# Kernel optimization log

Hardware: AMD Instinct MI355X
Metric: run time of the kernel (lower is better)

The kernel has to match this reference:

```python
import jax, jax.numpy as jnp
import numpy as np

N, F, T, E, TS, H = 10000, 64, 8, 160000, 200, 128
K = max(1, int(N * 0.5))
EPS = 1e-8


def layer_norm(x, g, b):
    m = x.mean(-1, keepdims=True)
    v = ((x - m) ** 2).mean(-1, keepdims=True)
    return (x - m) * jax.lax.rsqrt(v + 1e-5) * g + b


def setup_inputs() -> dict:
    key = jax.random.key(0)
    ks = jax.random.split(key, 16)
    s = lambda i, shape, scale=0.05: jax.random.normal(ks[i], shape, jnp.float32) * scale
    return {
        "x_seq": jax.random.normal(ks[0], (T, N, F), jnp.float32),
        "h0": jnp.zeros((N, H), jnp.float32),
        "c0": jnp.zeros((N, H), jnp.float32),
        "time_series": jax.random.normal(ks[1], (TS, N), jnp.float32),
        "Wx": s(2, (4, H, F)),            # gate order: input, forget, output, modulation
        "bx": jnp.zeros((4, H), jnp.float32),
        "Wh": s(3, (4, H, H)),
        "bh": jnp.zeros((4, H), jnp.float32),
        "ln_mod_g": jnp.ones((H,), jnp.float32),
        "ln_mod_b": jnp.zeros((H,), jnp.float32),
        "map_W": s(4, (3, H, H)),         # p1_i0, p2_i0, p2_i1
        "pool_vec": jax.random.normal(ks[5], (H, 1), jnp.float32),
        "lstm_Wih": s(6, (4 * H, N), 0.01),
        "lstm_Whh": s(7, (4 * H, H)),
        "lstm_bih": jnp.zeros((4 * H,), jnp.float32),
        "lstm_bhh": jnp.zeros((4 * H,), jnp.float32),
        "mlp_W1": s(8, (H, 2 * H)),
        "mlp_b1": jnp.zeros((H,), jnp.float32),
        "mlp_ln_g": jnp.ones((H,), jnp.float32),
        "mlp_ln_b": jnp.zeros((H,), jnp.float32),
        "mlp_W2": s(9, (H // 2, H)),
        "mlp_b2": jnp.zeros((H // 2,), jnp.float32),
        "mlp_W3": s(10, (1, H // 2)),
        "mlp_b3": jnp.zeros((1,), jnp.float32),
        "edge_index": jax.random.randint(ks[11], (2, E), 0, N, jnp.int32),
    }


def _forward(x_seq, h0, c0, time_series, Wx, bx, Wh, bh, ln_mod_g, ln_mod_b,
             map_W, pool_vec, lstm_Wih, lstm_Whh, lstm_bih, lstm_bhh,
             mlp_W1, mlp_b1, mlp_ln_g, mlp_ln_b, mlp_W2, mlp_b2, mlp_W3, mlp_b3,
             edge_index):
    src, dst = edge_index[0], edge_index[1]
    # GCN symmetric norm with self-loops: D^{-1/2}(A+I)D^{-1/2}
    deg = 1.0 + jax.ops.segment_sum(jnp.ones((E,), jnp.float32), dst, num_segments=N)
    dis = jax.lax.rsqrt(deg)
    enorm = dis[src] * dis[dst]
    self_norm = dis * dis

    def aggregate(hfeat):  # one shared gather/scatter for all 4 gates, [N, 4H]
        out = jax.ops.segment_sum(hfeat[src] * enorm[:, None], dst, num_segments=N)
        return out + hfeat * self_norm[:, None]

    bias = (bx + bh).reshape(4 * H)

    def cell(x, h, c):
        lin = (jnp.einsum('nf,ghf->ngh', x, Wx).reshape(N, 4 * H)
               + jnp.einsum('nd,ghd->ngh', h, Wh).reshape(N, 4 * H))
        pre = (aggregate(lin) + bias).reshape(N, 4, H)  # aggregation is linear -> fuse x- and h-branches
        i = jax.nn.relu(pre[:, 0])
        f = jax.nn.relu(pre[:, 1])
        o = jax.nn.relu(pre[:, 2])
        g = jnp.tanh(layer_norm(pre[:, 3], ln_mod_g, ln_mod_b))
        c_new = f * c + i * g
        return o * jnp.tanh(c_new), c_new

    # jump_connection_parallel over strides p in {1, 2}
    last = []
    for p in (1, 2):
        for off in range(p):
            h, c = h0, c0
            for t in range(off, T, p):
                h, c = cell(x_seq[t], h, c)
            last.append(h)
    hidden = sum(last[j] @ map_W[j].T for j in range(3))  # p1_i0 + p2_i0 + p2_i1

    # DGPool
    v = pool_vec / (jnp.linalg.norm(pool_vec) + EPS)
    sc = (hidden @ v).squeeze(-1)
    sc = (sc - sc.mean()) / (sc.std() + EPS)
    sig = jax.nn.sigmoid(sc)
    x_scaled = hidden * sig[:, None]
    _, idx = jax.lax.top_k(sig, K)
    new_x = x_scaled[idx]
    ss = -jnp.sort(-sig)
    pool_loss = -(jnp.log(ss[:K] + EPS).sum() + jnp.log(1.0 - ss[K:] + EPS).sum()) / N
    high = new_x.mean(axis=0)

    # raw time-series LSTM (torch gate order i, f, g, o)
    def step(carry, x_t):
        hh, cc = carry
        z = lstm_Wih @ x_t + lstm_bih + lstm_Whh @ hh + lstm_bhh
        i_, f_, g_, o_ = jnp.split(z, 4)
        cc = jax.nn.sigmoid(f_) * cc + jax.nn.sigmoid(i_) * jnp.tanh(g_)
        return (jax.nn.sigmoid(o_) * jnp.tanh(cc), cc), None

    (h_last, _), _ = jax.lax.scan(step, (jnp.zeros(H, jnp.float32), jnp.zeros(H, jnp.float32)), time_series)

    fusion = jnp.concatenate([high, h_last])
    m = jax.nn.relu(mlp_W1 @ fusion + mlp_b1)
    m = layer_norm(m, mlp_ln_g, mlp_ln_b)      # dropout = identity (eval mode)
    m = jax.nn.relu(mlp_W2 @ m + mlp_b2)
    pred = mlp_W3 @ m + mlp_b3
    return pred, pool_loss


def reference(x_seq, h0, c0, time_series, Wx, bx, Wh, bh, ln_mod_g, ln_mod_b,
              map_W, pool_vec, lstm_Wih, lstm_Whh, lstm_bih, lstm_bhh,
              mlp_W1, mlp_b1, mlp_ln_g, mlp_ln_b, mlp_W2, mlp_b2, mlp_W3, mlp_b3,
              edge_index):
    return _forward(x_seq, h0, c0, time_series, Wx, bx, Wh, bh, ln_mod_g, ln_mod_b,
                    map_W, pool_vec, lstm_Wih, lstm_Whh, lstm_bih, lstm_bhh,
                    mlp_W1, mlp_b1, mlp_ln_g, mlp_ln_b, mlp_W2, mlp_b2, mlp_W3, mlp_b3,
                    edge_index)
```

## Files before the change

### kernel.cpp

```cpp
#include <hip/hip_runtime.h>
#include <hip/hip_bf16.h>
#include <math.h>

#define NN 10000
#define FF 64
#define TSTEPS 8
#define EE 160000
#define TSS 200
#define HH 128
#define KK 5000
#define G4 512
#define KIN 192
#define EPSF 1e-8f

typedef __attribute__((ext_vector_type(8))) short short8v;
typedef __attribute__((ext_vector_type(4))) float f32x4;

__device__ inline float wred(float v){
  #pragma unroll
  for (int off = 32; off > 0; off >>= 1) v += __shfl_xor(v, off);
  return v;
}

__device__ inline unsigned short f2b(float f) {
  union { __hip_bfloat16 h; unsigned short u; } cv;
  cv.h = __float2bfloat16(f);
  return cv.u;
}
__device__ inline float b2f(unsigned short u) {
  return __uint_as_float(((unsigned int)u) << 16);
}


__global__ void k_setup_w(const float* Wx, const float* Wh, const float* bx, const float* bh,
                          const float* mapW, unsigned short* Wfrag, float* biasC, float* mapWr) {
  int idx = blockIdx.x * 256 + threadIdx.x;
  {
    int jj = idx & 7, l = (idx >> 3) & 63, ntg = (idx >> 9) & 31, ks = idx >> 14;
    int k = ks * 32 + ((l >> 4) << 3) + jj;
    int gh = ntg * 16 + (l & 15);
    int g = gh >> 7, hh = gh & 127;
    float v = (k < FF) ? Wx[(g * HH + hh) * FF + k] : Wh[(g * HH + hh) * HH + (k - FF)];
    Wfrag[idx] = f2b(v);
  }
  if (idx < G4) biasC[idx] = bx[idx] + bh[idx];
  if (idx < 3 * HH * HH) {
    int s = idx / (HH * HH), r = idx % (HH * HH);
    int d = r / HH, j = r % HH;
    mapWr[idx] = mapW[(s * HH + j) * HH + d];
  }
}

__global__ void k_zero(int* deg, int* cursor, int* rank, float* acc, float* high) {
  int i = blockIdx.x * 256 + threadIdx.x;
  if (i < NN) { deg[i] = 0; cursor[i] = 0; rank[i] = 0; }
  if (i < 16) acc[i] = 0.f;
  if (i < 128) high[i] = 0.f;
}

__global__ void k_deg(const int* ei, int* deg) {
  int e = blockIdx.x * 256 + threadIdx.x;
  if (e < EE) atomicAdd(&deg[ei[EE + e]], 1);
}

__global__ void k_norm(const int* deg, float* dis, float* self_norm) {
  int n = blockIdx.x * 256 + threadIdx.x;
  if (n < NN) {
    float d = 1.0f + (float)deg[n];
    dis[n] = rsqrtf(d);
    self_norm[n] = 1.0f / d;
  }
}

__global__ void k_scan(const int* deg, int* row_ptr, int n) {
  __shared__ int buf[1024];
  __shared__ int carry;
  if (threadIdx.x == 0) carry = 0;
  __syncthreads();
  for (int base = 0; base < n; base += 1024) {
    int i = base + threadIdx.x;
    int v = (i < n) ? deg[i] : 0;
    buf[threadIdx.x] = v;
    __syncthreads();
    for (int off = 1; off < 1024; off <<= 1) {
      int t = (threadIdx.x >= off) ? buf[threadIdx.x - off] : 0;
      __syncthreads();
      buf[threadIdx.x] += t;
      __syncthreads();
    }
    if (i < n) row_ptr[i] = carry + buf[threadIdx.x] - v;
    __syncthreads();
    if (threadIdx.x == 1023) carry += buf[1023];
    __syncthreads();
  }
  if (threadIdx.x == 0) row_ptr[n] = carry;
}

__global__ void k_fill(const int* ei, const int* row_ptr, int* cursor, const float* dis,
                       int* col_src, float* col_w) {
  int e = blockIdx.x * 256 + threadIdx.x;
  if (e < EE) {
    int s = ei[e], d = ei[EE + e];
    int pos = row_ptr[d] + atomicAdd(&cursor[d], 1);
    col_src[pos] = s;
    col_w[pos] = dis[s] * dis[d];
  }
}

__global__ void k_init3(const float* h0, const float* c0, unsigned short* hAll, float* cAll) {
  int i = blockIdx.x * 256 + threadIdx.x;
  if (i < NN * HH) {
    unsigned short h = f2b(h0[i]);
    float c = c0[i];
    hAll[i] = h; hAll[NN * HH + i] = h; hAll[2 * NN * HH + i] = h;
    cAll[i] = c; cAll[NN * HH + i] = c; cAll[2 * NN * HH + i] = c;
  }
}

__global__ void k_xcast(const float* x, unsigned short* xb) {
  int i = blockIdx.x * 256 + threadIdx.x;
  float4 v = *(const float4*)(x + (size_t)i * 4);
  ushort4 u;
  u.x = f2b(v.x); u.y = f2b(v.y); u.z = f2b(v.z); u.w = f2b(v.w);
  *(ushort4*)(xb + (size_t)i * 4) = u;
}


__global__ void __launch_bounds__(256) k_aggx8(const unsigned short* xb, const int* row_ptr,
    const int* col_src, const float* col_w, const float* self_n, unsigned short* aggX) {
  __shared__ int es[4][64];
  __shared__ float ew[4][64];
  int wv = threadIdx.x >> 6, lane = threadIdx.x & 63;
  int p = blockIdx.x * 4 + wv;
  int t = p / NN, n = p - t * NN;
  int e0 = row_ptr[n], e1 = row_ptr[n + 1];
  float acc = 0.f;
  for (int eb = e0; eb < e1; eb += 64) {
    int cnt = min(64, e1 - eb);
    if (lane < cnt) { es[wv][lane] = col_src[eb + lane]; ew[wv][lane] = col_w[eb + lane]; }
    __builtin_amdgcn_wave_barrier();
    for (int i = 0; i < cnt; i++)
      acc += b2f(xb[((size_t)t * NN + es[wv][i]) * FF + lane]) * ew[wv][i];
    __builtin_amdgcn_wave_barrier();
  }
  acc += b2f(xb[((size_t)t * NN + n) * FF + lane]) * self_n[n];
  aggX[(size_t)p * FF + lane] = f2b(acc);
}

__global__ void __launch_bounds__(256) k_aggh(const unsigned short* hAll, const int* row_ptr,
    const int* col_src, const float* col_w, const float* self_n, unsigned short* aggH, int M) {
  __shared__ int es[4][64];
  __shared__ float ew[4][64];
  int w = threadIdx.x >> 6, lane = threadIdx.x & 63;
  int m = blockIdx.x * 2 + (w >> 1);
  if (m >= M) return;
  int ch = (w & 1) * 64 + lane;
  int c = (m >= 2 * NN) ? 2 : (m >= NN ? 1 : 0);
  int n = m - c * NN;
  int e0 = row_ptr[n], e1 = row_ptr[n + 1];
  const unsigned short* hb = hAll + (size_t)c * NN * HH;
  float acc = 0.f;
  for (int eb = e0; eb < e1; eb += 64) {
    int cnt = min(64, e1 - eb);
    if (lane < cnt) { es[w][lane] = col_src[eb + lane]; ew[w][lane] = col_w[eb + lane]; }
    __builtin_amdgcn_wave_barrier();
    for (int i = 0; i < cnt; i++)
      acc += b2f(hb[(size_t)es[w][i] * HH + ch]) * ew[w][i];
    __builtin_amdgcn_wave_barrier();
  }
  acc += b2f(hAll[(size_t)m * HH + ch]) * self_n[n];
  aggH[(size_t)m * HH + ch] = f2b(acc);
}

__global__ void __launch_bounds__(512) k_premm(const unsigned short* aggX,
    const unsigned short* aggH, const unsigned short* Wfrag, const float* biasC,
    unsigned short* preB, int M, int r) {
  __shared__ unsigned short Af[1536 * 8];
  int m0 = blockIdx.x * 64;
  int n0 = blockIdx.y * 256;
  int tid = threadIdx.x;
  int l = tid & 63, wid = tid >> 6;
  int wm = wid >> 2, wn = wid & 3;
  #pragma unroll
  for (int q = 0; q < 3; q++) {
    int chunk = tid + q * 512;
    int mt = chunk / 384, rem = chunk - mt * 384;
    int ks = rem >> 6, cl = rem & 63;
    int row = m0 + mt * 16 + (cl & 15);
    int kk = ks * 32 + ((cl >> 4) << 3);
    short8v v = {};
    if (row < M) {
      const unsigned short* src;
      if (kk < FF) {
        int ch = (row >= 2 * NN) ? 2 : (row >= NN ? 1 : 0);
        int n = row - ch * NN;
        int t = (ch == 0) ? r : (2 * r + ch - 1);
        src = aggX + ((size_t)t * NN + n) * FF + kk;
      } else {
        src = aggH + (size_t)row * HH + (kk - FF);
      }
      v = *(const short8v*)src;
    }
    *(short8v*)&Af[chunk * 8] = v;
  }
  __syncthreads();
  f32x4 acc[2][4];
  #pragma unroll
  for (int i = 0; i < 2; i++)
    #pragma unroll
    for (int j = 0; j < 4; j++) acc[i][j] = (f32x4){0.f, 0.f, 0.f, 0.f};
  #pragma unroll
  for (int ks = 0; ks < 6; ks++) {
    short8v a0 = *(const short8v*)&Af[(((wm * 2 + 0) * 6 + ks) * 64 + l) * 8];
    short8v a1 = *(const short8v*)&Af[(((wm * 2 + 1) * 6 + ks) * 64 + l) * 8];
    #pragma unroll
    for (int j = 0; j < 4; j++) {
      int ntg = (n0 >> 4) + wn * 4 + j;
      short8v b = *(const short8v*)(Wfrag + (((size_t)ks * 32 + ntg) * 64 + l) * 8);
      acc[0][j] = __builtin_amdgcn_mfma_f32_16x16x32_bf16(a0, b, acc[0][j], 0, 0, 0);
      acc[1][j] = __builtin_amdgcn_mfma_f32_16x16x32_bf16(a1, b, acc[1][j], 0, 0, 0);
    }
  }
  #pragma unroll
  for (int i = 0; i < 2; i++)
    #pragma unroll
    for (int j = 0; j < 4; j++) {
      int colg = n0 + wn * 64 + j * 16 + (l & 15);
      float bv = biasC[colg];
      #pragma unroll
      for (int rg = 0; rg < 4; rg++) {
        int row = m0 + wm * 32 + i * 16 + ((l >> 4) * 4) + rg;
        if (row < M) preB[(size_t)row * G4 + colg] = f2b(acc[i][j][rg] + bv);
      }
    }
}

__global__ void __launch_bounds__(128) k_gates(const unsigned short* preB, const float* lng,
                                               const float* lnb, unsigned short* h, float* c,
                                               int M) {
  int b = blockIdx.x;
  int j = threadIdx.x;
  const unsigned short* p = preB + (size_t)b * G4;
  float iv = b2f(p[j]), fv = b2f(p[128 + j]), ov = b2f(p[256 + j]), gv = b2f(p[384 + j]);
  float s = wred(gv), s2 = wred(gv * gv);
  __shared__ float sh[4];
  int wid = j >> 6;
  if ((j & 63) == 0) { sh[wid] = s; sh[2 + wid] = s2; }
  __syncthreads();
  float mean = (sh[0] + sh[1]) * (1.f / 128.f);
  float var = (sh[2] + sh[3]) * (1.f / 128.f) - mean * mean;
  float gn = (gv - mean) * rsqrtf(var + 1e-5f) * lng[j] + lnb[j];
  float gt = tanhf(gn);
  float ii = fmaxf(iv, 0.f), ff = fmaxf(fv, 0.f), oo = fmaxf(ov, 0.f);
  size_t ci = (size_t)b * HH + j;
  float cn = ff * c[ci] + ii * gt;
  c[ci] = cn;
  h[ci] = f2b(oo * tanhf(cn));
}

__global__ void __launch_bounds__(256) k_hidden(const unsigned short* hA, const unsigned short* hB,
                                                const unsigned short* hC, const float* Wr,
                                                float* out) {
  __shared__ __align__(16) float As[8][128];
  __shared__ __align__(16) float Bs[8][64];
  int m0 = blockIdx.x * 128, n0 = blockIdx.y * 64;
  int tid = threadIdx.x;
  int tx = tid & 15, ty = tid >> 4;
  float acc[8][4] = {};
  for (int kc = 0; kc < 48; kc++) {
    int k0 = kc * 8;
    const unsigned short* S = (k0 < 128) ? hA : (k0 < 256 ? hB : hC);
    int koff = k0 & 127;
    {
      int ml = tid >> 1, kq = (tid & 1) * 4;
      int m = m0 + ml;
      float4 v = make_float4(0.f, 0.f, 0.f, 0.f);
      if (m < NN) {
        ushort4 u = *(const ushort4*)(S + (size_t)m * HH + koff + kq);
        v.x = b2f(u.x); v.y = b2f(u.y); v.z = b2f(u.z); v.w = b2f(u.w);
      }
      As[kq + 0][ml] = v.x; As[kq + 1][ml] = v.y; As[kq + 2][ml] = v.z; As[kq + 3][ml] = v.w;
    }
    #pragma unroll
    for (int q = 0; q < 2; q++) {
      int e = tid + q * 256;
      int kl = e >> 6, nl = e & 63;
      Bs[kl][nl] = Wr[(size_t)(k0 + kl) * HH + n0 + nl];
    }
    __syncthreads();
    #pragma unroll
    for (int k = 0; k < 8; k++) {
      float4 a0 = *(const float4*)&As[k][ty * 4];
      float4 a1 = *(const float4*)&As[k][64 + ty * 4];
      float4 b0 = *(const float4*)&Bs[k][tx * 4];
      const float av0[4] = {a0.x, a0.y, a0.z, a0.w};
      const float av1[4] = {a1.x, a1.y, a1.z, a1.w};
      const float bv[4] = {b0.x, b0.y, b0.z, b0.w};
      #pragma unroll
      for (int i = 0; i < 4; i++)
        #pragma unroll
        for (int j = 0; j < 4; j++) {
          acc[i][j] += av0[i] * bv[j];
          acc[4 + i][j] += av1[i] * bv[j];
        }
    }
    __syncthreads();
  }
  #pragma unroll
  for (int g = 0; g < 2; g++)
    #pragma unroll
    for (int i = 0; i < 4; i++) {
      int m = m0 + g * 64 + ty * 4 + i;
      if (m < NN) {
        float4 r;
        r.x = acc[g * 4 + i][0]; r.y = acc[g * 4 + i][1];
        r.z = acc[g * 4 + i][2]; r.w = acc[g * 4 + i][3];
        *(float4*)(out + (size_t)m * HH + n0 + tx * 4) = r;
      }
    }
}


__global__ void k_vnorm(const float* pv, float* acc) {
  int t = threadIdx.x;
  float v = pv[t];
  float s = wred(v * v);
  __shared__ float sh[2];
  if ((t & 63) == 0) sh[t >> 6] = s;
  __syncthreads();
  if (t == 0) acc[0] = 1.0f / (sqrtf(sh[0] + sh[1]) + EPSF);
}

__global__ void __launch_bounds__(256) k_sc(const float* hidden, const float* pv, float* acc,
                                            float* sc) {
  int wid = threadIdx.x >> 6, lane = threadIdx.x & 63;
  float2 vv = *(const float2*)(pv + lane * 2);
  float inv = acc[0];
  float ls = 0.f, ls2 = 0.f;
  for (int n = blockIdx.x * 4 + wid; n < NN; n += gridDim.x * 4) {
    float2 hv = *(const float2*)(hidden + (size_t)n * HH + lane * 2);
    float dot = hv.x * vv.x + hv.y * vv.y;
    dot = wred(dot);
    if (lane == 0) {
      float s = dot * inv;
      sc[n] = s;
      ls += s;
      ls2 += s * s;
    }
  }
  __shared__ float sh[8];
  if (lane == 0) { sh[wid] = ls; sh[4 + wid] = ls2; }
  __syncthreads();
  if (threadIdx.x == 0) {
    atomicAdd(&acc[1], sh[0] + sh[1] + sh[2] + sh[3]);
    atomicAdd(&acc[2], sh[4] + sh[5] + sh[6] + sh[7]);
  }
}

__global__ void k_sig(const float* sc, const float* acc, float* sig) {
  int n = blockIdx.x * 256 + threadIdx.x;
  if (n < NN) {
    float mean = acc[1] * (1.f / NN);
    float var = acc[2] * (1.f / NN) - mean * mean;
    float sd = sqrtf(fmaxf(var, 0.f)) + EPSF;
    float z = (sc[n] - mean) / sd;
    sig[n] = 1.f / (1.f + expf(-z));
  }
}

__global__ void __launch_bounds__(256) k_rank(const float* sc, int* rank) {
  __shared__ float sj[1024];
  int i = blockIdx.x * 256 + threadIdx.x;
  int j0 = blockIdx.y * 1024;
  for (int k = threadIdx.x; k < 1024; k += 256) {
    int j = j0 + k;
    sj[k] = (j < NN) ? sc[j] : -3.0e38f;
  }
  __syncthreads();
  float si = (i < NN) ? sc[i] : 0.f;
  int jmax = NN - j0; if (jmax > 1024) jmax = 1024;
  int cnt = 0;
  for (int k = 0; k < jmax; k++) {
    float v = sj[k];
    int j = j0 + k;
    cnt += (v > si) || (v == si && j < i);
  }
  if (i < NN && cnt) atomicAdd(&rank[i], cnt);
}

__global__ void __launch_bounds__(256) k_plogs(const float* sig, const int* rank, float* acc) {
  int i = blockIdx.x * 256 + threadIdx.x;
  float v = 0.f;
  if (i < NN) {
    float s = sig[i];
    v = (rank[i] < KK) ? logf(s + EPSF) : logf(1.f - s + EPSF);
  }
  v = wred(v);
  __shared__ float sh[4];
  if ((threadIdx.x & 63) == 0) sh[threadIdx.x >> 6] = v;
  __syncthreads();
  if (threadIdx.x == 0) atomicAdd(&acc[3], sh[0] + sh[1] + sh[2] + sh[3]);
}

__global__ void __launch_bounds__(128) k_high(const float* hidden, const float* sig,
                                              const int* rank, float* high) {
  int ch = threadIdx.x;
  int n0 = blockIdx.x * 128;
  float a = 0.f;
  for (int q = 0; q < 128; q++) {
    int n = n0 + q;
    if (n >= NN) break;
    if (rank[n] < KK) a += hidden[(size_t)n * HH + ch] * sig[n];
  }
  atomicAdd(&high[ch], a);
}


__global__ void __launch_bounds__(256) k_zpre2(const float* Wih, const float* ts, float* part) {
  __shared__ __align__(16) float As[16][64];
  __shared__ __align__(16) float Bs[16][64];
  int m0 = blockIdx.x * 64;
  int n0 = blockIdx.y * 64;
  int ks = blockIdx.z;
  int kbeg = ks * 624;
  int kend = (ks == 15) ? NN : kbeg + 624;
  int tid = threadIdx.x;
  int tx = tid & 15, ty = tid >> 4;
  int lm = tid >> 2, kq = (tid & 3) * 4;
  bool bvalid = (n0 + lm) < TSS;
  float acc[4][4] = {};
  for (int k0 = kbeg; k0 < kend; k0 += 16) {
    {
      float4 v = *(const float4*)(Wih + (size_t)(m0 + lm) * NN + k0 + kq);
      As[kq + 0][lm] = v.x; As[kq + 1][lm] = v.y; As[kq + 2][lm] = v.z; As[kq + 3][lm] = v.w;
    }
    {
      float4 v = make_float4(0.f, 0.f, 0.f, 0.f);
      if (bvalid) v = *(const float4*)(ts + (size_t)(n0 + lm) * NN + k0 + kq);
      Bs[kq + 0][lm] = v.x; Bs[kq + 1][lm] = v.y; Bs[kq + 2][lm] = v.z; Bs[kq + 3][lm] = v.w;
    }
    __syncthreads();
    #pragma unroll
    for (int k = 0; k < 16; k++) {
      float4 a0 = *(const float4*)&As[k][ty * 4];
      float4 b0 = *(const float4*)&Bs[k][tx * 4];
      const float av[4] = {a0.x, a0.y, a0.z, a0.w};
      const float bv[4] = {b0.x, b0.y, b0.z, b0.w};
      #pragma unroll
      for (int i = 0; i < 4; i++)
        #pragma unroll
        for (int j = 0; j < 4; j++)
          acc[i][j] += av[i] * bv[j];
    }
    __syncthreads();
  }
  float* pd = part + ((size_t)ks << 17);
  #pragma unroll
  for (int i = 0; i < 4; i++) {
    float4 r4 = make_float4(acc[i][0], acc[i][1], acc[i][2], acc[i][3]);
    *(float4*)(pd + (size_t)(m0 + ty * 4 + i) * 256 + n0 + tx * 4) = r4;
  }
}

__global__ void __launch_bounds__(256) k_zred(const float* part, float* zpre) {
  int r = blockIdx.x;
  int t = threadIdx.x;
  int base = r * 256 + t;
  float s = 0.f;
  #pragma unroll
  for (int k = 0; k < 16; k++) s += part[(k << 17) + base];
  if (t < TSS) zpre[(size_t)t * G4 + r] = s;
}

__global__ void __launch_bounds__(1024) k_lstm(const float* Whh, const float* bih, const float* bhh,
                                               const float* zpre, float* h_last) {
  __shared__ float part[2][512];
  __shared__ float gact[512];
  int tid = threadIdx.x;
  int half = tid >> 9;
  int r = tid & 511;
  int w = tid >> 6, l = tid & 63;
  float w64[64];
  #pragma unroll
  for (int q = 0; q < 16; q++) {
    float4 v = *(const float4*)(Whh + (size_t)r * HH + 64 * half + 4 * q);
    w64[4 * q + 0] = v.x; w64[4 * q + 1] = v.y;
    w64[4 * q + 2] = v.z; w64[4 * q + 3] = v.w;
  }
  float bias = bih[r] + bhh[r];
  int jbase = (w >= 8) ? 64 : 0;
  float hreg = 0.f, creg = 0.f;
  for (int t = 0; t < TSS; t++) {
    float d = 0.f;
    #pragma unroll
    for (int j = 0; j < 64; j++) {
      float hj = __uint_as_float(__builtin_amdgcn_readlane(__float_as_uint(hreg), j));
      d += w64[j] * hj;
    }
    part[half][r] = d;
    __syncthreads();
    if (tid < 512) {
      float dd = part[0][r] + part[1][r] + bias + zpre[(size_t)t * G4 + r];
      float a = ((r >> 7) == 2) ? tanhf(dd) : (1.f / (1.f + expf(-dd)));
      gact[r] = a;
    }
    __syncthreads();
    int j = jbase + l;
    creg = gact[128 + j] * creg + gact[j] * gact[256 + j];
    hreg = gact[384 + j] * tanhf(creg);
  }
  if (w == 0) h_last[l] = hreg;
  else if (w == 8) h_last[64 + l] = hreg;
}


__global__ void __launch_bounds__(256) k_mlp(const float* high, const float* hlast, const float* acc,
    const float* W1, const float* b1, const float* lng, const float* lnb,
    const float* W2, const float* b2, const float* W3, const float* b3, float* out) {
  __shared__ float fus[256];
  __shared__ float m1[128];
  __shared__ float m2[64];
  __shared__ float red[4];
  int t = threadIdx.x;
  fus[t] = (t < 128) ? high[t] * (1.f / KK) : hlast[t - 128];
  __syncthreads();
  if (t < 128) {
    float a = b1[t];
    for (int k = 0; k < 256; k++) a += W1[t * 256 + k] * fus[k];
    m1[t] = fmaxf(a, 0.f);
  }
  __syncthreads();
  if (t < 128) {
    float x = m1[t];
    float s = wred(x), s2 = wred(x * x);
    if ((t & 63) == 0) { red[t >> 6] = s; red[2 + (t >> 6)] = s2; }
  }
  __syncthreads();
  if (t < 128) {
    float mean = (red[0] + red[1]) * (1.f / 128.f);
    float var = (red[2] + red[3]) * (1.f / 128.f) - mean * mean;
    float xn = (m1[t] - mean) * rsqrtf(var + 1e-5f) * lng[t] + lnb[t];
    __syncthreads();
    m1[t] = xn;
  } else {
    __syncthreads();
  }
  __syncthreads();
  if (t < 64) {
    float a = b2[t];
    for (int k = 0; k < 128; k++) a += W2[t * 128 + k] * m1[k];
    m2[t] = fmaxf(a, 0.f);
  }
  __syncthreads();
  if (t < 64) {
    float a = W3[t] * m2[t];
    a = wred(a);
    if (t == 0) {
      out[0] = a + b3[0];
      out[1] = -acc[3] * (1.f / NN);
    }
  }
}


extern "C" void kernel_launch(void* const* d_in, const int* in_sizes, int n_in,
                              void* d_out, int out_size, void* d_ws, size_t ws_size,
                              hipStream_t stream) {
  const float* x_seq = (const float*)d_in[0];
  const float* h0    = (const float*)d_in[1];
  const float* c0    = (const float*)d_in[2];
  const float* ts    = (const float*)d_in[3];
  const float* Wx    = (const float*)d_in[4];
  const float* bx    = (const float*)d_in[5];
  const float* Wh    = (const float*)d_in[6];
  const float* bh    = (const float*)d_in[7];
  const float* lng   = (const float*)d_in[8];
  const float* lnb   = (const float*)d_in[9];
  const float* mapW  = (const float*)d_in[10];
  const float* pv    = (const float*)d_in[11];
  const float* Wih   = (const float*)d_in[12];
  const float* Whh   = (const float*)d_in[13];
  const float* bih   = (const float*)d_in[14];
  const float* bhh   = (const float*)d_in[15];
  const float* W1    = (const float*)d_in[16];
  const float* b1    = (const float*)d_in[17];
  const float* mlng  = (const float*)d_in[18];
  const float* mlnb  = (const float*)d_in[19];
  const float* W2    = (const float*)d_in[20];
  const float* b2    = (const float*)d_in[21];
  const float* W3    = (const float*)d_in[22];
  const float* b3    = (const float*)d_in[23];
  const int*   ei    = (const int*)d_in[24];

  char* wsp = (char*)d_ws;
  size_t off = 0;
  auto carve = [&](size_t bytes) -> char* {
    char* p = wsp + off;
    off += (bytes + 255) & ~(size_t)255;
    return p;
  };
  unsigned short* Wfrag = (unsigned short*)carve(98304 * 2);
  float* biasC   = (float*)carve(G4 * 4);
  float* mapWr   = (float*)carve(3 * HH * HH * 4);
  int*   degi    = (int*)carve(NN * 4);
  int*   cursor  = (int*)carve(NN * 4);
  int*   rankb   = (int*)carve(NN * 4);
  int*   row_ptr = (int*)carve((NN + 1) * 4);
  float* dis     = (float*)carve(NN * 4);
  float* self_n  = (float*)carve(NN * 4);
  int*   col_src = (int*)carve(EE * 4);
  float* col_w   = (float*)carve(EE * 4);
  unsigned short* hAll = (unsigned short*)carve((size_t)3 * NN * HH * 2);
  float*          cAll = (float*)carve((size_t)3 * NN * HH * 4);
  unsigned short* x2b  = (unsigned short*)carve((size_t)TSTEPS * NN * FF * 2);
  unsigned short* aggX = (unsigned short*)carve((size_t)TSTEPS * NN * FF * 2);
  unsigned short* aggH = (unsigned short*)carve((size_t)3 * NN * HH * 2);
  unsigned short* preB = (unsigned short*)carve((size_t)3 * NN * G4 * 2);
  float* hidden  = (float*)carve((size_t)NN * HH * 4);
  float* sc      = (float*)carve(NN * 4);
  float* sig     = (float*)carve(NN * 4);
  float* acc     = (float*)carve(16 * 4);
  float* high    = (float*)carve(128 * 4);
  float* zpre    = (float*)carve((size_t)TSS * G4 * 4);
  float* hlast   = (float*)carve(128 * 4);

  k_setup_w<<<384, 256, 0, stream>>>(Wx, Wh, bx, bh, mapW, Wfrag, biasC, mapWr);
  k_zero<<<40, 256, 0, stream>>>(degi, cursor, rankb, acc, high);
  k_deg<<<625, 256, 0, stream>>>(ei, degi);
  k_norm<<<40, 256, 0, stream>>>(degi, dis, self_n);
  k_scan<<<1, 1024, 0, stream>>>(degi, row_ptr, NN);
  k_fill<<<625, 256, 0, stream>>>(ei, row_ptr, cursor, dis, col_src, col_w);
  k_init3<<<5000, 256, 0, stream>>>(h0, c0, hAll, cAll);
  k_xcast<<<5000, 256, 0, stream>>>(x_seq, x2b);

  k_aggx8<<<20000, 256, 0, stream>>>(x2b, row_ptr, col_src, col_w, self_n, aggX);

  for (int r = 0; r < TSTEPS; r++) {
    int M = (r < 4) ? 3 * NN : NN;
    k_aggh<<<M / 2, 256, 0, stream>>>(hAll, row_ptr, col_src, col_w, self_n, aggH, M);
    k_premm<<<dim3((M + 63) / 64, 2), 512, 0, stream>>>(aggX, aggH, Wfrag, biasC, preB, M, r);
    k_gates<<<M, 128, 0, stream>>>(preB, lng, lnb, hAll, cAll, M);
  }

  k_hidden<<<dim3(79, 2), 256, 0, stream>>>(hAll, hAll + (size_t)NN * HH,
                                            hAll + (size_t)2 * NN * HH, mapWr, hidden);
  k_vnorm<<<1, 128, 0, stream>>>(pv, acc);
  k_sc<<<250, 256, 0, stream>>>(hidden, pv, acc, sc);
  k_sig<<<40, 256, 0, stream>>>(sc, acc, sig);
  k_rank<<<dim3(40, 10), 256, 0, stream>>>(sc, rankb);
  k_plogs<<<40, 256, 0, stream>>>(sig, rankb, acc);
  k_high<<<79, 128, 0, stream>>>(hidden, sig, rankb, high);

  k_zpre2<<<dim3(8, 4, 16), 256, 0, stream>>>(Wih, ts, (float*)preB);
  k_zred<<<512, 256, 0, stream>>>((float*)preB, zpre);
  k_lstm<<<1, 1024, 0, stream>>>(Whh, bih, bhh, zpre, hlast);

  k_mlp<<<1, 256, 0, stream>>>(high, hlast, acc, W1, b1, mlng, mlnb, W2, b2, W3, b3,
                               (float*)d_out);
}
```

Measured before the change: 1.177 ms.

## Restructure serial LSTM kernel to one thread per gate row with full-row weights

The sequential LSTM recurrence kernel now uses 512 threads, and each thread holds a full 128-wide row of Whh in registers, instead of 1024 threads each holding a half row. This removes the shared-memory partial-sum exchange and one reduction step per timestep. The cell/hidden update now runs on 128 threads and broadcasts h through shared memory. The dot product is split into four independent FMA chains to add ILP. The cost is higher register pressure (128 weight floats per thread) and a serial cell update on two waves, while the block still needs two barriers per step.

```diff
diff --git a/kernel.cpp b/kernel.cpp
--- a/kernel.cpp
+++ b/kernel.cpp
@@ -472,45 +472,52 @@
   if (t < TSS) zpre[(size_t)t * G4 + r] = s;
 }
 
-__global__ void __launch_bounds__(1024) k_lstm(const float* Whh, const float* bih, const float* bhh,
-                                               const float* zpre, float* h_last) {
-  __shared__ float part[2][512];
+#define RLN(x, J) __uint_as_float(__builtin_amdgcn_readlane(__float_as_uint(x), (J)))
+#define MAC4(Q, HR, B, D) \
+  D = fmaf(wv##Q.x, RLN(HR, (B) + 0), D); \
+  D = fmaf(wv##Q.y, RLN(HR, (B) + 1), D); \
+  D = fmaf(wv##Q.z, RLN(HR, (B) + 2), D); \
+  D = fmaf(wv##Q.w, RLN(HR, (B) + 3), D);
+#define LDW(Q) float4 wv##Q = *(const float4*)(wr + 4 * Q);
+
+__global__ void __launch_bounds__(512) k_lstm(const float* Whh, const float* bih, const float* bhh,
+                                              const float* zpre, float* h_last) {
   __shared__ float gact[512];
-  int tid = threadIdx.x;
-  int half = tid >> 9;
-  int r = tid & 511;
-  int w = tid >> 6, l = tid & 63;
-  float w64[64];
-  #pragma unroll
-  for (int q = 0; q < 16; q++) {
-    float4 v = *(const float4*)(Whh + (size_t)r * HH + 64 * half + 4 * q);
-    w64[4 * q + 0] = v.x; w64[4 * q + 1] = v.y;
-    w64[4 * q + 2] = v.z; w64[4 * q + 3] = v.w;
-  }
+  __shared__ float hs[128];
+  int r = threadIdx.x;
+  int l = r & 63;
+  const float* wr = Whh + (size_t)r * HH;
+  LDW(0) LDW(1) LDW(2) LDW(3) LDW(4) LDW(5) LDW(6) LDW(7)
+  LDW(8) LDW(9) LDW(10) LDW(11) LDW(12) LDW(13) LDW(14) LDW(15)
+  LDW(16) LDW(17) LDW(18) LDW(19) LDW(20) LDW(21) LDW(22) LDW(23)
+  LDW(24) LDW(25) LDW(26) LDW(27) LDW(28) LDW(29) LDW(30) LDW(31)
   float bias = bih[r] + bhh[r];
-  int jbase = (w >= 8) ? 64 : 0;
-  float hreg = 0.f, creg = 0.f;
+  float hreg0 = 0.f, hreg1 = 0.f, creg = 0.f;
+  int gate = r >> 7;
   for (int t = 0; t < TSS; t++) {
-    float d = 0.f;
-    #pragma unroll
-    for (int j = 0; j < 64; j++) {
-      float hj = __uint_as_float(__builtin_amdgcn_readlane(__float_as_uint(hreg), j));
-      d += w64[j] * hj;
-    }
-    part[half][r] = d;
-    __syncthreads();
-    if (tid < 512) {
-      float dd = part[0][r] + part[1][r] + bias + zpre[(size_t)t * G4 + r];
-      float a = ((r >> 7) == 2) ? tanhf(dd) : (1.f / (1.f + expf(-dd)));
-      gact[r] = a;
-    }
-    __syncthreads();
-    int j = jbase + l;
-    creg = gact[128 + j] * creg + gact[j] * gact[256 + j];
-    hreg = gact[384 + j] * tanhf(creg);
-  }
-  if (w == 0) h_last[l] = hreg;
-  else if (w == 8) h_last[64 + l] = hreg;
+    float z = zpre[(size_t)t * G4 + r];
+    float d0 = 0.f, d1 = 0.f, d2 = 0.f, d3 = 0.f;
+    MAC4(0, hreg0, 0, d0)  MAC4(1, hreg0, 4, d1)  MAC4(2, hreg0, 8, d2)  MAC4(3, hreg0, 12, d3)
+    MAC4(4, hreg0, 16, d0) MAC4(5, hreg0, 20, d1) MAC4(6, hreg0, 24, d2) MAC4(7, hreg0, 28, d3)
+    MAC4(8, hreg0, 32, d0) MAC4(9, hreg0, 36, d1) MAC4(10, hreg0, 40, d2) MAC4(11, hreg0, 44, d3)
+    MAC4(12, hreg0, 48, d0) MAC4(13, hreg0, 52, d1) MAC4(14, hreg0, 56, d2) MAC4(15, hreg0, 60, d3)
+    MAC4(16, hreg1, 0, d0)  MAC4(17, hreg1, 4, d1)  MAC4(18, hreg1, 8, d2)  MAC4(19, hreg1, 12, d3)
+    MAC4(20, hreg1, 16, d0) MAC4(21, hreg1, 20, d1) MAC4(22, hreg1, 24, d2) MAC4(23, hreg1, 28, d3)
+    MAC4(24, hreg1, 32, d0) MAC4(25, hreg1, 36, d1) MAC4(26, hreg1, 40, d2) MAC4(27, hreg1, 44, d3)
+    MAC4(28, hreg1, 48, d0) MAC4(29, hreg1, 52, d1) MAC4(30, hreg1, 56, d2) MAC4(31, hreg1, 60, d3)
+    float d = ((d0 + d1) + (d2 + d3)) + bias + z;
+    float a = (gate == 2) ? tanhf(d) : (1.f / (1.f + expf(-d)));
+    gact[r] = a;
+    __syncthreads();
+    if (r < 128) {
+      creg = gact[128 + r] * creg + gact[r] * gact[256 + r];
+      hs[r] = gact[384 + r] * tanhf(creg);
+    }
+    __syncthreads();
+    hreg0 = hs[l];
+    hreg1 = hs[64 + l];
+  }
+  if (r < 128) h_last[r] = hs[r];
 }
 
 
@@ -653,7 +660,7 @@
 
   k_zpre2<<<dim3(8, 4, 16), 256, 0, stream>>>(Wih, ts, (float*)preB);
   k_zred<<<512, 256, 0, stream>>>((float*)preB, zpre);
-  k_lstm<<<1, 1024, 0, stream>>>(Whh, bih, bhh, zpre, hlast);
+  k_lstm<<<1, 512, 0, stream>>>(Whh, bih, bhh, zpre, hlast);
 
   k_mlp<<<1, 256, 0, stream>>>(high, hlast, acc, W1, b1, mlng, mlnb, W2, b2, W3, b3,
                                (float*)d_out);
```

New measurement: 1.107 ms. -5.9%, faster.
